# Performance work log

Measured on AMD Instinct MI355X. Metric: run time of the kernel, lower is better.

Reference implementation:

```python
import math
import jax, jax.numpy as jnp
import numpy as np

jax.config.update("jax_enable_x64", True)  # hash math uses int64, as in the torch reference

N_LEVELS = 16
F = 2                     # n_feat_per_entry
T = 2 ** 19               # hashmap size per level (max)
BASE_RES = 16
MAX_RES = 512
MIN_XYZ = -0.75           # origin (0,0,0), side 1.5
MAX_XYZ = 0.75
B = 1_000_000

# per_level_scale computed in float32 like torch.exp(torch.log(...))
_SCALE = float(np.exp(np.log(np.float32(MAX_RES / BASE_RES)) / np.float32(N_LEVELS - 1)))

def _level_info():
    offsets, res, n = [], [], 0
    for i in range(N_LEVELS):
        offsets.append(n)
        r = math.floor(BASE_RES * _SCALE ** i)
        res.append(r)
        n += min(T, (r + 1) ** 3)
    offsets.append(n)
    return offsets, res, n

OFFSETS, RES, N_TOTAL = _level_info()  # N_TOTAL == 5262476
PRIMES = np.array([1, 2654435761, 805459861], dtype=np.int64)
# corner offsets in {0,1}^3; weight = prod over dims of (frac if corner==1 else 1-frac)
CORNERS = np.array([[i, j, k] for i in (0, 1) for j in (0, 1) for k in (0, 1)], dtype=np.int64)  # (8,3)


def _hashgrid_forward(xyz, embeddings):
    """xyz: (B,3) float32 inside the bbox; embeddings: (N_TOTAL,F) float32."""
    norm = (xyz - MIN_XYZ) / (MAX_XYZ - MIN_XYZ)  # (B,3) in [0,1]
    corners = jnp.asarray(CORNERS)                # (8,3) int64
    primes = jnp.asarray(PRIMES)                  # (3,) int64
    corner_is_one = jnp.asarray(CORNERS.astype(bool))  # (8,3)
    outs = [xyz]  # include_input=True, raw input first
    for lvl in range(N_LEVELS):
        r = RES[lvl]
        off = OFFSETS[lvl]
        size = OFFSETS[lvl + 1] - off   # = min(T, (r+1)^3)
        pos = norm * r                                     # (B,3)
        base = jnp.clip(jnp.floor(pos).astype(jnp.int64), 0, r - 1)  # (B,3)
        frac = pos - base.astype(pos.dtype)                # (B,3)
        idx3 = base[:, None, :] + corners[None]            # (B,8,3) grid-pt coords
        # fast_hash: xor of coord*prime per dim, then mod level size, plus level offset
        p = idx3 * primes                                  # (B,8,3) int64
        hidx = (p[..., 0] ^ p[..., 1] ^ p[..., 2]) % size + off  # (B,8)
        vals = embeddings[hidx]                            # (B,8,F) gather
        w = jnp.prod(jnp.where(corner_is_one[None], frac[:, None, :], 1.0 - frac[:, None, :]), axis=-1)  # (B,8)
        outs.append(jnp.einsum('bc,bcf->bf', w, vals))     # trilinear interp -> (B,F)
    return jnp.concatenate(outs, axis=-1)                  # (B, 3 + L*F) = (B,35)


def setup_inputs() -> dict:
    key = jax.random.key(0)
    k1, k2 = jax.random.split(key)
    # points strictly inside the bbox [-0.75, 0.75]^3
    xyz = jax.random.uniform(k1, (B, 3), dtype=jnp.float32,
                             minval=MIN_XYZ + 1e-3, maxval=MAX_XYZ - 1e-3)
    # torch init is uniform(-1e-4, 1e-4)
    emb = jax.random.uniform(k2, (N_TOTAL, F), dtype=jnp.float32, minval=-1e-4, maxval=1e-4)
    return {"xyz": xyz, "embeddings": emb}


def reference(xyz, embeddings):
    return _hashgrid_forward(xyz, embeddings)
```

## Files before the change

### kernel.cpp

```cpp
#include <hip/hip_runtime.h>
#include <stdint.h>
#include <string.h>

#define NLEV 16

typedef float  vfloat4 __attribute__((ext_vector_type(4)));

__device__ __forceinline__ void norm_coords(const float* __restrict__ xyz, int p,
                                            float& nx, float& ny, float& nz) {
    const float x = __builtin_nontemporal_load(xyz + 3 * p + 0);
    const float y = __builtin_nontemporal_load(xyz + 3 * p + 1);
    const float z = __builtin_nontemporal_load(xyz + 3 * p + 2);
    const float inv = 1.0f / 1.5f;
    nx = (x + 0.75f) * inv;
    ny = (y + 0.75f) * inv;
    nz = (z + 0.75f) * inv;
}

__device__ __forceinline__ float2 trilerp(const float2 v[8],
                                          float fx, float fy, float fz) {
    const float gx = 1.0f - fx, gy = 1.0f - fy, gz = 1.0f - fz;
    const float w00 = gx * gy, w01 = gx * fy, w10 = fx * gy, w11 = fx * fy;
    float w, f0, f1;
    w = w00 * gz; f0 = w * v[0].x;          f1 = w * v[0].y;
    w = w00 * fz; f0 = fmaf(w, v[1].x, f0); f1 = fmaf(w, v[1].y, f1);
    w = w01 * gz; f0 = fmaf(w, v[2].x, f0); f1 = fmaf(w, v[2].y, f1);
    w = w01 * fz; f0 = fmaf(w, v[3].x, f0); f1 = fmaf(w, v[3].y, f1);
    w = w10 * gz; f0 = fmaf(w, v[4].x, f0); f1 = fmaf(w, v[4].y, f1);
    w = w10 * fz; f0 = fmaf(w, v[5].x, f0); f1 = fmaf(w, v[5].y, f1);
    w = w11 * gz; f0 = fmaf(w, v[6].x, f0); f1 = fmaf(w, v[6].y, f1);
    w = w11 * fz; f0 = fmaf(w, v[7].x, f0); f1 = fmaf(w, v[7].y, f1);
    return make_float2(f0, f1);
}

template<int R, uint32_t OFF>
__global__ __launch_bounds__(256, 4) void big_level2(
    const float* __restrict__ xyz,
    const float2* __restrict__ emb,
    float2* __restrict__ ws,
    int nb)
{
    const int t  = threadIdx.x;
    const int p0 = blockIdx.x * 512 + t;
    const int p1 = p0 + 256;
    const int q[2] = { p0 < nb ? p0 : nb - 1, p1 < nb ? p1 : nb - 1 };

    const float4* __restrict__ emb4 = (const float4*)emb;
    const uint32_t M = 524287u;

    uint32_t h0[2][4];
    uint32_t yzs[2][4];
    uint32_t hx1_[2];
    float4   V[2][4];
    float2   w1[2][4];
    float    fx[2], fy[2], fz[2];
    bool     oddbx[2];

    #pragma unroll
    for (int j = 0; j < 2; ++j) {
        float nx, ny, nz;
        norm_coords(xyz, q[j], nx, ny, nz);
        const float rf = (float)R;
        const float px = nx * rf, py = ny * rf, pz = nz * rf;
        int bx = (int)floorf(px); bx = bx < 0 ? 0 : (bx > R - 1 ? R - 1 : bx);
        int by = (int)floorf(py); by = by < 0 ? 0 : (by > R - 1 ? R - 1 : by);
        int bz = (int)floorf(pz); bz = bz < 0 ? 0 : (bz > R - 1 ? R - 1 : bz);
        fx[j] = px - (float)bx;
        fy[j] = py - (float)by;
        fz[j] = pz - (float)bz;

        const uint32_t hy0 = (uint32_t)by       * 2654435761u;
        const uint32_t hy1 = (uint32_t)(by + 1) * 2654435761u;
        const uint32_t hz0 = (uint32_t)bz       * 805459861u;
        const uint32_t hz1 = (uint32_t)(bz + 1) * 805459861u;
        yzs[j][0] = hy0 ^ hz0; yzs[j][1] = hy0 ^ hz1;
        yzs[j][2] = hy1 ^ hz0; yzs[j][3] = hy1 ^ hz1;

        const uint32_t hx0 = (uint32_t)bx;
        oddbx[j] = (bx & 1) != 0;
        hx1_[j]  = hx0 + 1u;

        #pragma unroll
        for (int i = 0; i < 4; ++i) {
            h0[j][i] = (hx0 ^ yzs[j][i]) & M;
            V[j][i]  = emb4[(h0[j][i] >> 1) + (OFF >> 1)];
        }
    }

    #pragma unroll
    for (int j = 0; j < 2; ++j) {
        if (oddbx[j]) {
            #pragma unroll
            for (int i = 0; i < 4; ++i)
                w1[j][i] = emb[((hx1_[j] ^ yzs[j][i]) & M) + OFF];
        }
    }

    float2 r[2];
    #pragma unroll
    for (int j = 0; j < 2; ++j) {
        float2 v[8];
        #pragma unroll
        for (int i = 0; i < 4; ++i) {
            const float2 lo = make_float2(V[j][i].x, V[j][i].y);
            const float2 hi = make_float2(V[j][i].z, V[j][i].w);
            const bool oh = (h0[j][i] & 1u) != 0u;
            v[i]     = oh ? hi : lo;
            v[i + 4] = oddbx[j] ? w1[j][i] : (oh ? lo : hi);
        }
        r[j] = trilerp(v, fx[j], fy[j], fz[j]);
    }

    uint64_t u0, u1;
    memcpy(&u0, &r[0], 8);
    memcpy(&u1, &r[1], 8);
    if (p0 < nb) __builtin_nontemporal_store(u0, (uint64_t*)ws + p0);
    if (p1 < nb) __builtin_nontemporal_store(u1, (uint64_t*)ws + p1);
}

__global__ __launch_bounds__(256, 4) void pack_small(
    const float* __restrict__ xyz,
    const float2* __restrict__ emb,
    const float2* __restrict__ ws,
    float* __restrict__ out,
    int nb)
{
    constexpr int      kRes[7]  = {16, 20, 25, 32, 40, 50, 64};
    constexpr uint32_t kSize[7] = {4913u, 9261u, 17576u, 35937u, 68921u, 132651u, 274625u};
    constexpr uint32_t kOff[7]  = {0u, 4913u, 14174u, 31750u, 67687u, 136608u, 269259u};

    __shared__ __align__(16) float lds[4 * 64 * 35];

    const int tid  = threadIdx.x;
    const int lane = tid & 63;
    const int wid  = tid >> 6;
    const int p    = blockIdx.x * 256 + tid;
    const int pc   = (p < nb) ? p : (nb - 1);

    uint64_t wsv[9];
    #pragma unroll
    for (int l = 0; l < 9; ++l)
        wsv[l] = __builtin_nontemporal_load(
            (const uint64_t*)ws + (size_t)l * nb + pc);

    const float x = xyz[3 * pc + 0];
    const float y = xyz[3 * pc + 1];
    const float z = xyz[3 * pc + 2];

    float* wl = &lds[(wid * 64 + lane) * 35];
    wl[0] = x; wl[1] = y; wl[2] = z;

    const float inv = 1.0f / 1.5f;
    const float nx = (x + 0.75f) * inv;
    const float ny = (y + 0.75f) * inv;
    const float nz = (z + 0.75f) * inv;

    uint32_t idx[2][8];
    float2   v[2][8];
    float    fr[2][3];

    auto level_idx = [&](int lv, uint32_t (&ix)[8], float (&f)[3]) {
        const int      r   = kRes[lv];
        const float    rf  = (float)r;
        const uint32_t sz  = kSize[lv];
        const uint32_t off = kOff[lv];

        const float px = nx * rf, py = ny * rf, pz = nz * rf;
        int bx = (int)floorf(px); bx = bx < 0 ? 0 : (bx > r - 1 ? r - 1 : bx);
        int by = (int)floorf(py); by = by < 0 ? 0 : (by > r - 1 ? r - 1 : by);
        int bz = (int)floorf(pz); bz = bz < 0 ? 0 : (bz > r - 1 ? r - 1 : bz);
        f[0] = px - (float)bx;
        f[1] = py - (float)by;
        f[2] = pz - (float)bz;

        const uint64_t hx0 = (uint64_t)(uint32_t)bx;
        const uint64_t hx1 = hx0 + 1u;
        const uint64_t hy0 = (uint64_t)(uint32_t)by       * 2654435761ull;
        const uint64_t hy1 = (uint64_t)(uint32_t)(by + 1) * 2654435761ull;
        const uint64_t hz0 = (uint64_t)(uint32_t)bz       * 805459861ull;
        const uint64_t hz1 = (uint64_t)(uint32_t)(bz + 1) * 805459861ull;

        const uint64_t yz00 = hy0 ^ hz0, yz01 = hy0 ^ hz1;
        const uint64_t yz10 = hy1 ^ hz0, yz11 = hy1 ^ hz1;

        ix[0] = (uint32_t)((hx0 ^ yz00) % sz) + off;
        ix[1] = (uint32_t)((hx0 ^ yz01) % sz) + off;
        ix[2] = (uint32_t)((hx0 ^ yz10) % sz) + off;
        ix[3] = (uint32_t)((hx0 ^ yz11) % sz) + off;
        ix[4] = (uint32_t)((hx1 ^ yz00) % sz) + off;
        ix[5] = (uint32_t)((hx1 ^ yz01) % sz) + off;
        ix[6] = (uint32_t)((hx1 ^ yz10) % sz) + off;
        ix[7] = (uint32_t)((hx1 ^ yz11) % sz) + off;
    };

    level_idx(0, idx[0], fr[0]);
    #pragma unroll
    for (int i = 0; i < 8; ++i) v[0][i] = emb[idx[0][i]];

    #pragma unroll
    for (int l = 0; l < 7; ++l) {
        const int cur = l & 1;
        const int nxt = cur ^ 1;
        if (l < 6) {
            level_idx(l + 1, idx[nxt], fr[nxt]);
            #pragma unroll
            for (int i = 0; i < 8; ++i) v[nxt][i] = emb[idx[nxt][i]];
        }
        const float2 rr = trilerp(v[cur], fr[cur][0], fr[cur][1], fr[cur][2]);
        wl[3 + 2 * l] = rr.x;
        wl[4 + 2 * l] = rr.y;
    }

    #pragma unroll
    for (int l = 0; l < 9; ++l) {
        float2 bv;
        memcpy(&bv, &wsv[l], 8);
        wl[3 + 2 * (l + 7)] = bv.x;
        wl[4 + 2 * (l + 7)] = bv.y;
    }

    __syncthreads();

    const int wave_gid = blockIdx.x * 4 + wid;
    if (wave_gid * 64 < nb) {
        const vfloat4* s4 = (const vfloat4*)&lds[wid * 64 * 35];
        vfloat4* d4 = (vfloat4*)(out + (size_t)wave_gid * (64 * 35));
        #pragma unroll
        for (int c = 0; c < 8; ++c)
            __builtin_nontemporal_store(s4[c * 64 + lane], &d4[c * 64 + lane]);
        if (lane < 48)
            __builtin_nontemporal_store(s4[8 * 64 + lane], &d4[8 * 64 + lane]);
    }
}

__global__ __launch_bounds__(256, 4) void hashgrid_mono(
    const float* __restrict__ xyz,
    const float2* __restrict__ emb,
    float* __restrict__ out,
    int nb)
{
    constexpr int      kRes[NLEV]  = {16,20,25,32,40,50,64,80,101,128,161,203,256,322,406,512};
    constexpr uint32_t kSize[NLEV] = {4913u,9261u,17576u,35937u,68921u,132651u,274625u,
                                      524288u,524288u,524288u,524288u,524288u,
                                      524288u,524288u,524288u,524288u};
    constexpr uint32_t kOff[NLEV]  = {0u,4913u,14174u,31750u,67687u,136608u,269259u,543884u,
                                      1068172u,1592460u,2116748u,2641036u,3165324u,
                                      3689612u,4213900u,4738188u};

    __shared__ __align__(16) float lds[4 * 64 * 35];

    const int tid  = threadIdx.x;
    const int lane = tid & 63;
    const int wid  = tid >> 6;
    const int p    = blockIdx.x * 256 + tid;
    const int pc   = (p < nb) ? p : (nb - 1);

    const float x = xyz[3 * pc + 0];
    const float y = xyz[3 * pc + 1];
    const float z = xyz[3 * pc + 2];

    float* wl = &lds[(wid * 64 + lane) * 35];
    wl[0] = x; wl[1] = y; wl[2] = z;

    const float inv = 1.0f / 1.5f;
    const float nx = (x + 0.75f) * inv;
    const float ny = (y + 0.75f) * inv;
    const float nz = (z + 0.75f) * inv;

    #pragma unroll
    for (int l = 0; l < NLEV; ++l) {
        const int      r   = kRes[l];
        const float    rf  = (float)r;
        const uint32_t sz  = kSize[l];
        const uint32_t off = kOff[l];

        const float px = nx * rf, py = ny * rf, pz = nz * rf;
        int bx = (int)floorf(px); bx = bx < 0 ? 0 : (bx > r - 1 ? r - 1 : bx);
        int by = (int)floorf(py); by = by < 0 ? 0 : (by > r - 1 ? r - 1 : by);
        int bz = (int)floorf(pz); bz = bz < 0 ? 0 : (bz > r - 1 ? r - 1 : bz);
        const float fx = px - (float)bx;
        const float fy = py - (float)by;
        const float fz = pz - (float)bz;

        const uint64_t hx0 = (uint64_t)(uint32_t)bx;
        const uint64_t hx1 = hx0 + 1u;
        const uint64_t hy0 = (uint64_t)(uint32_t)by       * 2654435761ull;
        const uint64_t hy1 = (uint64_t)(uint32_t)(by + 1) * 2654435761ull;
        const uint64_t hz0 = (uint64_t)(uint32_t)bz       * 805459861ull;
        const uint64_t hz1 = (uint64_t)(uint32_t)(bz + 1) * 805459861ull;

        const uint64_t yz00 = hy0 ^ hz0, yz01 = hy0 ^ hz1;
        const uint64_t yz10 = hy1 ^ hz0, yz11 = hy1 ^ hz1;

        const uint32_t i000 = (uint32_t)((hx0 ^ yz00) % sz) + off;
        const uint32_t i001 = (uint32_t)((hx0 ^ yz01) % sz) + off;
        const uint32_t i010 = (uint32_t)((hx0 ^ yz10) % sz) + off;
        const uint32_t i011 = (uint32_t)((hx0 ^ yz11) % sz) + off;
        const uint32_t i100 = (uint32_t)((hx1 ^ yz00) % sz) + off;
        const uint32_t i101 = (uint32_t)((hx1 ^ yz01) % sz) + off;
        const uint32_t i110 = (uint32_t)((hx1 ^ yz10) % sz) + off;
        const uint32_t i111 = (uint32_t)((hx1 ^ yz11) % sz) + off;

        const float2 v000 = emb[i000];
        const float2 v001 = emb[i001];
        const float2 v010 = emb[i010];
        const float2 v011 = emb[i011];
        const float2 v100 = emb[i100];
        const float2 v101 = emb[i101];
        const float2 v110 = emb[i110];
        const float2 v111 = emb[i111];

        const float gx = 1.0f - fx, gy = 1.0f - fy, gz = 1.0f - fz;
        const float w00 = gx * gy, w01 = gx * fy, w10 = fx * gy, w11 = fx * fy;

        float w, f0, f1;
        w = w00 * gz; f0 = w * v000.x;          f1 = w * v000.y;
        w = w00 * fz; f0 = fmaf(w, v001.x, f0); f1 = fmaf(w, v001.y, f1);
        w = w01 * gz; f0 = fmaf(w, v010.x, f0); f1 = fmaf(w, v010.y, f1);
        w = w01 * fz; f0 = fmaf(w, v011.x, f0); f1 = fmaf(w, v011.y, f1);
        w = w10 * gz; f0 = fmaf(w, v100.x, f0); f1 = fmaf(w, v100.y, f1);
        w = w10 * fz; f0 = fmaf(w, v101.x, f0); f1 = fmaf(w, v101.y, f1);
        w = w11 * gz; f0 = fmaf(w, v110.x, f0); f1 = fmaf(w, v110.y, f1);
        w = w11 * fz; f0 = fmaf(w, v111.x, f0); f1 = fmaf(w, v111.y, f1);

        wl[3 + 2 * l] = f0;
        wl[4 + 2 * l] = f1;
    }

    __syncthreads();

    const int wave_gid = blockIdx.x * 4 + wid;
    if (wave_gid * 64 < nb) {
        const float* src = &lds[wid * 64 * 35];
        float* dst = out + (size_t)wave_gid * (64 * 35);
        #pragma unroll
        for (int c = 0; c < 35; ++c)
            dst[c * 64 + lane] = src[c * 64 + lane];
    }
}

extern "C" void kernel_launch(void* const* d_in, const int* in_sizes, int n_in,
                              void* d_out, int out_size, void* d_ws, size_t ws_size,
                              hipStream_t stream) {
    const float*  xyz = (const float*)d_in[0];
    const float2* emb = (const float2*)d_in[1];
    float*        out = (float*)d_out;
    const int nb = in_sizes[0] / 3;
    const int blocks  = (nb + 255) / 256;
    const int blocks2 = (nb + 511) / 512;

    const size_t ws_need = (size_t)9 * (size_t)nb * sizeof(float2);
    if (ws_size < ws_need) {
        hashgrid_mono<<<blocks, 256, 0, stream>>>(xyz, emb, out, nb);
        return;
    }

    float2* ws = (float2*)d_ws;
    big_level2< 80,  543884u><<<blocks2, 256, 0, stream>>>(xyz, emb, ws + (size_t)0 * nb, nb);
    big_level2<101, 1068172u><<<blocks2, 256, 0, stream>>>(xyz, emb, ws + (size_t)1 * nb, nb);
    big_level2<128, 1592460u><<<blocks2, 256, 0, stream>>>(xyz, emb, ws + (size_t)2 * nb, nb);
    big_level2<161, 2116748u><<<blocks2, 256, 0, stream>>>(xyz, emb, ws + (size_t)3 * nb, nb);
    big_level2<203, 2641036u><<<blocks2, 256, 0, stream>>>(xyz, emb, ws + (size_t)4 * nb, nb);
    big_level2<256, 3165324u><<<blocks2, 256, 0, stream>>>(xyz, emb, ws + (size_t)5 * nb, nb);
    big_level2<322, 3689612u><<<blocks2, 256, 0, stream>>>(xyz, emb, ws + (size_t)6 * nb, nb);
    big_level2<406, 4213900u><<<blocks2, 256, 0, stream>>>(xyz, emb, ws + (size_t)7 * nb, nb);
    big_level2<512, 4738188u><<<blocks2, 256, 0, stream>>>(xyz, emb, ws + (size_t)8 * nb, nb);
    pack_small<<<blocks, 256, 0, stream>>>(xyz, emb, ws, out, nb);
}
```

Measured before the change: 625.2 us.

## Process four points per thread in big-level kernels and deepen small-level prefetch

```diff
diff --git a/kernel.cpp b/kernel.cpp
--- a/kernel.cpp
+++ b/kernel.cpp
@@ -33,92 +33,112 @@
     return make_float2(f0, f1);
 }
 
+struct BigPt {
+    uint32_t h0[4];
+    uint32_t yzs[4];
+    uint32_t hx1;
+    bool     oddbx;
+    float    fx, fy, fz;
+    float4   V[4];
+    float2   w1[4];
+};
+
 template<int R, uint32_t OFF>
-__global__ __launch_bounds__(256, 4) void big_level2(
+__device__ __forceinline__ void big_issue(const float4* __restrict__ emb4,
+                                          const float2* __restrict__ emb,
+                                          float nx, float ny, float nz, BigPt& s) {
+    const uint32_t M = 524287u;
+    const float rf = (float)R;
+    const float px = nx * rf, py = ny * rf, pz = nz * rf;
+    int bx = (int)floorf(px); bx = bx < 0 ? 0 : (bx > R - 1 ? R - 1 : bx);
+    int by = (int)floorf(py); by = by < 0 ? 0 : (by > R - 1 ? R - 1 : by);
+    int bz = (int)floorf(pz); bz = bz < 0 ? 0 : (bz > R - 1 ? R - 1 : bz);
+    s.fx = px - (float)bx;
+    s.fy = py - (float)by;
+    s.fz = pz - (float)bz;
+
+    const uint32_t hy0 = (uint32_t)by       * 2654435761u;
+    const uint32_t hy1 = (uint32_t)(by + 1) * 2654435761u;
+    const uint32_t hz0 = (uint32_t)bz       * 805459861u;
+    const uint32_t hz1 = (uint32_t)(bz + 1) * 805459861u;
+    s.yzs[0] = hy0 ^ hz0; s.yzs[1] = hy0 ^ hz1;
+    s.yzs[2] = hy1 ^ hz0; s.yzs[3] = hy1 ^ hz1;
+
+    const uint32_t hx0 = (uint32_t)bx;
+    s.oddbx = (bx & 1) != 0;
+    s.hx1   = hx0 + 1u;
+
+    #pragma unroll
+    for (int i = 0; i < 4; ++i) {
+        s.h0[i] = (hx0 ^ s.yzs[i]) & M;
+        s.V[i]  = emb4[(s.h0[i] >> 1) + (OFF >> 1)];
+    }
+    if (s.oddbx) {
+        #pragma unroll
+        for (int i = 0; i < 4; ++i)
+            s.w1[i] = emb[((s.hx1 ^ s.yzs[i]) & M) + OFF];
+    }
+}
+
+__device__ __forceinline__ float2 big_consume(const BigPt& s) {
+    float2 v[8];
+    #pragma unroll
+    for (int i = 0; i < 4; ++i) {
+        const float2 lo = make_float2(s.V[i].x, s.V[i].y);
+        const float2 hi = make_float2(s.V[i].z, s.V[i].w);
+        const bool oh = (s.h0[i] & 1u) != 0u;
+        v[i]     = oh ? hi : lo;
+        v[i + 4] = s.oddbx ? s.w1[i] : (oh ? lo : hi);
+    }
+    return trilerp(v, s.fx, s.fy, s.fz);
+}
+
+template<int R, uint32_t OFF>
+__global__ __launch_bounds__(256, 4) void big_level4(
     const float* __restrict__ xyz,
     const float2* __restrict__ emb,
     float2* __restrict__ ws,
     int nb)
 {
-    const int t  = threadIdx.x;
-    const int p0 = blockIdx.x * 512 + t;
-    const int p1 = p0 + 256;
-    const int q[2] = { p0 < nb ? p0 : nb - 1, p1 < nb ? p1 : nb - 1 };
-
+    const int t    = threadIdx.x;
+    const int base = blockIdx.x * 1024 + t;
     const float4* __restrict__ emb4 = (const float4*)emb;
-    const uint32_t M = 524287u;
-
-    uint32_t h0[2][4];
-    uint32_t yzs[2][4];
-    uint32_t hx1_[2];
-    float4   V[2][4];
-    float2   w1[2][4];
-    float    fx[2], fy[2], fz[2];
-    bool     oddbx[2];
-
-    #pragma unroll
-    for (int j = 0; j < 2; ++j) {
-        float nx, ny, nz;
-        norm_coords(xyz, q[j], nx, ny, nz);
-        const float rf = (float)R;
-        const float px = nx * rf, py = ny * rf, pz = nz * rf;
-        int bx = (int)floorf(px); bx = bx < 0 ? 0 : (bx > R - 1 ? R - 1 : bx);
-        int by = (int)floorf(py); by = by < 0 ? 0 : (by > R - 1 ? R - 1 : by);
-        int bz = (int)floorf(pz); bz = bz < 0 ? 0 : (bz > R - 1 ? R - 1 : bz);
-        fx[j] = px - (float)bx;
-        fy[j] = py - (float)by;
-        fz[j] = pz - (float)bz;
-
-        const uint32_t hy0 = (uint32_t)by       * 2654435761u;
-        const uint32_t hy1 = (uint32_t)(by + 1) * 2654435761u;
-        const uint32_t hz0 = (uint32_t)bz       * 805459861u;
-        const uint32_t hz1 = (uint32_t)(bz + 1) * 805459861u;
-        yzs[j][0] = hy0 ^ hz0; yzs[j][1] = hy0 ^ hz1;
-        yzs[j][2] = hy1 ^ hz0; yzs[j][3] = hy1 ^ hz1;
-
-        const uint32_t hx0 = (uint32_t)bx;
-        oddbx[j] = (bx & 1) != 0;
-        hx1_[j]  = hx0 + 1u;
-
-        #pragma unroll
-        for (int i = 0; i < 4; ++i) {
-            h0[j][i] = (hx0 ^ yzs[j][i]) & M;
-            V[j][i]  = emb4[(h0[j][i] >> 1) + (OFF >> 1)];
-        }
-    }
-
-    #pragma unroll
-    for (int j = 0; j < 2; ++j) {
-        if (oddbx[j]) {
-            #pragma unroll
-            for (int i = 0; i < 4; ++i)
-                w1[j][i] = emb[((hx1_[j] ^ yzs[j][i]) & M) + OFF];
-        }
-    }
-
-    float2 r[2];
-    #pragma unroll
-    for (int j = 0; j < 2; ++j) {
-        float2 v[8];
-        #pragma unroll
-        for (int i = 0; i < 4; ++i) {
-            const float2 lo = make_float2(V[j][i].x, V[j][i].y);
-            const float2 hi = make_float2(V[j][i].z, V[j][i].w);
-            const bool oh = (h0[j][i] & 1u) != 0u;
-            v[i]     = oh ? hi : lo;
-            v[i + 4] = oddbx[j] ? w1[j][i] : (oh ? lo : hi);
-        }
-        r[j] = trilerp(v, fx[j], fy[j], fz[j]);
-    }
-
-    uint64_t u0, u1;
-    memcpy(&u0, &r[0], 8);
-    memcpy(&u1, &r[1], 8);
+
+    int p0 = base, p1 = base + 256, p2 = base + 512, p3 = base + 768;
+    const int q0 = p0 < nb ? p0 : nb - 1;
+    const int q1 = p1 < nb ? p1 : nb - 1;
+    const int q2 = p2 < nb ? p2 : nb - 1;
+    const int q3 = p3 < nb ? p3 : nb - 1;
+
+    float nx0, ny0, nz0, nx1, ny1, nz1, nx2, ny2, nz2, nx3, ny3, nz3;
+    norm_coords(xyz, q0, nx0, ny0, nz0);
+    norm_coords(xyz, q1, nx1, ny1, nz1);
+    norm_coords(xyz, q2, nx2, ny2, nz2);
+    norm_coords(xyz, q3, nx3, ny3, nz3);
+
+    BigPt s0, s1, s2, s3;
+    big_issue<R, OFF>(emb4, emb, nx0, ny0, nz0, s0);
+    big_issue<R, OFF>(emb4, emb, nx1, ny1, nz1, s1);
+    big_issue<R, OFF>(emb4, emb, nx2, ny2, nz2, s2);
+
+    const float2 r0 = big_consume(s0);
+    big_issue<R, OFF>(emb4, emb, nx3, ny3, nz3, s3);
+    const float2 r1 = big_consume(s1);
+    const float2 r2 = big_consume(s2);
+    const float2 r3 = big_consume(s3);
+
+    uint64_t u0, u1, u2, u3;
+    memcpy(&u0, &r0, 8);
+    memcpy(&u1, &r1, 8);
+    memcpy(&u2, &r2, 8);
+    memcpy(&u3, &r3, 8);
     if (p0 < nb) __builtin_nontemporal_store(u0, (uint64_t*)ws + p0);
     if (p1 < nb) __builtin_nontemporal_store(u1, (uint64_t*)ws + p1);
-}
-
-__global__ __launch_bounds__(256, 4) void pack_small(
+    if (p2 < nb) __builtin_nontemporal_store(u2, (uint64_t*)ws + p2);
+    if (p3 < nb) __builtin_nontemporal_store(u3, (uint64_t*)ws + p3);
+}
+
+__global__ __launch_bounds__(64, 4) void pack_small(
     const float* __restrict__ xyz,
     const float2* __restrict__ emb,
     const float2* __restrict__ ws,
@@ -129,12 +149,10 @@
     constexpr uint32_t kSize[7] = {4913u, 9261u, 17576u, 35937u, 68921u, 132651u, 274625u};
     constexpr uint32_t kOff[7]  = {0u, 4913u, 14174u, 31750u, 67687u, 136608u, 269259u};
 
-    __shared__ __align__(16) float lds[4 * 64 * 35];
-
-    const int tid  = threadIdx.x;
-    const int lane = tid & 63;
-    const int wid  = tid >> 6;
-    const int p    = blockIdx.x * 256 + tid;
+    __shared__ __align__(16) float lds[64 * 35];
+
+    const int lane = threadIdx.x;
+    const int p    = blockIdx.x * 64 + lane;
     const int pc   = (p < nb) ? p : (nb - 1);
 
     uint64_t wsv[9];
@@ -147,7 +165,7 @@
     const float y = xyz[3 * pc + 1];
     const float z = xyz[3 * pc + 2];
 
-    float* wl = &lds[(wid * 64 + lane) * 35];
+    float* wl = &lds[lane * 35];
     wl[0] = x; wl[1] = y; wl[2] = z;
 
     const float inv = 1.0f / 1.5f;
@@ -155,9 +173,9 @@
     const float ny = (y + 0.75f) * inv;
     const float nz = (z + 0.75f) * inv;
 
-    uint32_t idx[2][8];
-    float2   v[2][8];
-    float    fr[2][3];
+    uint32_t idx[3][8];
+    float2   v[3][8];
+    float    fr[3][3];
 
     auto level_idx = [&](int lv, uint32_t (&ix)[8], float (&f)[3]) {
         const int      r   = kRes[lv];
@@ -196,13 +214,16 @@
     level_idx(0, idx[0], fr[0]);
     #pragma unroll
     for (int i = 0; i < 8; ++i) v[0][i] = emb[idx[0][i]];
+    level_idx(1, idx[1], fr[1]);
+    #pragma unroll
+    for (int i = 0; i < 8; ++i) v[1][i] = emb[idx[1][i]];
 
     #pragma unroll
     for (int l = 0; l < 7; ++l) {
-        const int cur = l & 1;
-        const int nxt = cur ^ 1;
-        if (l < 6) {
-            level_idx(l + 1, idx[nxt], fr[nxt]);
+        const int cur = l % 3;
+        if (l < 5) {
+            const int nxt = (l + 2) % 3;
+            level_idx(l + 2, idx[nxt], fr[nxt]);
             #pragma unroll
             for (int i = 0; i < 8; ++i) v[nxt][i] = emb[idx[nxt][i]];
         }
@@ -221,10 +242,9 @@
 
     __syncthreads();
 
-    const int wave_gid = blockIdx.x * 4 + wid;
-    if (wave_gid * 64 < nb) {
-        const vfloat4* s4 = (const vfloat4*)&lds[wid * 64 * 35];
-        vfloat4* d4 = (vfloat4*)(out + (size_t)wave_gid * (64 * 35));
+    if (blockIdx.x * 64 < nb) {
+        const vfloat4* s4 = (const vfloat4*)lds;
+        vfloat4* d4 = (vfloat4*)(out + (size_t)blockIdx.x * (64 * 35));
         #pragma unroll
         for (int c = 0; c < 8; ++c)
             __builtin_nontemporal_store(s4[c * 64 + lane], &d4[c * 64 + lane]);
@@ -346,24 +366,25 @@
     const float2* emb = (const float2*)d_in[1];
     float*        out = (float*)d_out;
     const int nb = in_sizes[0] / 3;
-    const int blocks  = (nb + 255) / 256;
-    const int blocks2 = (nb + 511) / 512;
+    const int blocksP = (nb + 63) / 64;
+    const int blocksB = (nb + 1023) / 1024;
 
     const size_t ws_need = (size_t)9 * (size_t)nb * sizeof(float2);
     if (ws_size < ws_need) {
-        hashgrid_mono<<<blocks, 256, 0, stream>>>(xyz, emb, out, nb);
+        const int blocksM = (nb + 255) / 256;
+        hashgrid_mono<<<blocksM, 256, 0, stream>>>(xyz, emb, out, nb);
         return;
     }
 
     float2* ws = (float2*)d_ws;
-    big_level2< 80,  543884u><<<blocks2, 256, 0, stream>>>(xyz, emb, ws + (size_t)0 * nb, nb);
-    big_level2<101, 1068172u><<<blocks2, 256, 0, stream>>>(xyz, emb, ws + (size_t)1 * nb, nb);
-    big_level2<128, 1592460u><<<blocks2, 256, 0, stream>>>(xyz, emb, ws + (size_t)2 * nb, nb);
-    big_level2<161, 2116748u><<<blocks2, 256, 0, stream>>>(xyz, emb, ws + (size_t)3 * nb, nb);
-    big_level2<203, 2641036u><<<blocks2, 256, 0, stream>>>(xyz, emb, ws + (size_t)4 * nb, nb);
-    big_level2<256, 3165324u><<<blocks2, 256, 0, stream>>>(xyz, emb, ws + (size_t)5 * nb, nb);
-    big_level2<322, 3689612u><<<blocks2, 256, 0, stream>>>(xyz, emb, ws + (size_t)6 * nb, nb);
-    big_level2<406, 4213900u><<<blocks2, 256, 0, stream>>>(xyz, emb, ws + (size_t)7 * nb, nb);
-    big_level2<512, 4738188u><<<blocks2, 256, 0, stream>>>(xyz, emb, ws + (size_t)8 * nb, nb);
-    pack_small<<<blocks, 256, 0, stream>>>(xyz, emb, ws, out, nb);
-}
+    big_level4< 80,  543884u><<<blocksB, 256, 0, stream>>>(xyz, emb, ws + (size_t)0 * nb, nb);
+    big_level4<101, 1068172u><<<blocksB, 256, 0, stream>>>(xyz, emb, ws + (size_t)1 * nb, nb);
+    big_level4<128, 1592460u><<<blocksB, 256, 0, stream>>>(xyz, emb, ws + (size_t)2 * nb, nb);
+    big_level4<161, 2116748u><<<blocksB, 256, 0, stream>>>(xyz, emb, ws + (size_t)3 * nb, nb);
+    big_level4<203, 2641036u><<<blocksB, 256, 0, stream>>>(xyz, emb, ws + (size_t)4 * nb, nb);
+    big_level4<256, 3165324u><<<blocksB, 256, 0, stream>>>(xyz, emb, ws + (size_t)5 * nb, nb);
+    big_level4<322, 3689612u><<<blocksB, 256, 0, stream>>>(xyz, emb, ws + (size_t)6 * nb, nb);
+    big_level4<406, 4213900u><<<blocksB, 256, 0, stream>>>(xyz, emb, ws + (size_t)7 * nb, nb);
+    big_level4<512, 4738188u><<<blocksB, 256, 0, stream>>>(xyz, emb, ws + (size_t)8 * nb, nb);
+    pack_small<<<blocksP, 64, 0, stream>>>(xyz, emb, ws, out, nb);
+}
```

Result: slower. 732.9 us (+17.2%).

## Pair x-adjacent hash corners into one 16-byte load for dense levels

Applied to the files above, without the earlier changes.

```diff
diff --git a/kernel.cpp b/kernel.cpp
--- a/kernel.cpp
+++ b/kernel.cpp
@@ -155,24 +155,22 @@
     const float ny = (y + 0.75f) * inv;
     const float nz = (z + 0.75f) * inv;
 
-    uint32_t idx[2][8];
-    float2   v[2][8];
-    float    fr[2][3];
-
-    auto level_idx = [&](int lv, uint32_t (&ix)[8], float (&f)[3]) {
-        const int      r   = kRes[lv];
+    #pragma unroll
+    for (int l = 0; l < 7; ++l) {
+        const int      r   = kRes[l];
         const float    rf  = (float)r;
-        const uint32_t sz  = kSize[lv];
-        const uint32_t off = kOff[lv];
+        const uint32_t sz  = kSize[l];
+        const uint32_t off = kOff[l];
 
         const float px = nx * rf, py = ny * rf, pz = nz * rf;
         int bx = (int)floorf(px); bx = bx < 0 ? 0 : (bx > r - 1 ? r - 1 : bx);
         int by = (int)floorf(py); by = by < 0 ? 0 : (by > r - 1 ? r - 1 : by);
         int bz = (int)floorf(pz); bz = bz < 0 ? 0 : (bz > r - 1 ? r - 1 : bz);
-        f[0] = px - (float)bx;
-        f[1] = py - (float)by;
-        f[2] = pz - (float)bz;
-
+        const float fx = px - (float)bx;
+        const float fy = py - (float)by;
+        const float fz = pz - (float)bz;
+
+        const bool     evenbx = (bx & 1) == 0;
         const uint64_t hx0 = (uint64_t)(uint32_t)bx;
         const uint64_t hx1 = hx0 + 1u;
         const uint64_t hy0 = (uint64_t)(uint32_t)by       * 2654435761ull;
@@ -180,33 +178,30 @@
         const uint64_t hz0 = (uint64_t)(uint32_t)bz       * 805459861ull;
         const uint64_t hz1 = (uint64_t)(uint32_t)(bz + 1) * 805459861ull;
 
-        const uint64_t yz00 = hy0 ^ hz0, yz01 = hy0 ^ hz1;
-        const uint64_t yz10 = hy1 ^ hz0, yz11 = hy1 ^ hz1;
-
-        ix[0] = (uint32_t)((hx0 ^ yz00) % sz) + off;
-        ix[1] = (uint32_t)((hx0 ^ yz01) % sz) + off;
-        ix[2] = (uint32_t)((hx0 ^ yz10) % sz) + off;
-        ix[3] = (uint32_t)((hx0 ^ yz11) % sz) + off;
-        ix[4] = (uint32_t)((hx1 ^ yz00) % sz) + off;
-        ix[5] = (uint32_t)((hx1 ^ yz01) % sz) + off;
-        ix[6] = (uint32_t)((hx1 ^ yz10) % sz) + off;
-        ix[7] = (uint32_t)((hx1 ^ yz11) % sz) + off;
-    };
-
-    level_idx(0, idx[0], fr[0]);
-    #pragma unroll
-    for (int i = 0; i < 8; ++i) v[0][i] = emb[idx[0][i]];
-
-    #pragma unroll
-    for (int l = 0; l < 7; ++l) {
-        const int cur = l & 1;
-        const int nxt = cur ^ 1;
-        if (l < 6) {
-            level_idx(l + 1, idx[nxt], fr[nxt]);
-            #pragma unroll
-            for (int i = 0; i < 8; ++i) v[nxt][i] = emb[idx[nxt][i]];
+        const uint64_t yzc[4] = { hy0 ^ hz0, hy0 ^ hz1, hy1 ^ hz0, hy1 ^ hz1 };
+
+        float2 v[8];
+        #pragma unroll
+        for (int c = 0; c < 4; ++c) {
+            const uint64_t a0 = hx0 ^ yzc[c];
+            const uint32_t h0 = (uint32_t)(a0 % sz);
+            const bool     odd_a = ((uint32_t)a0 & 1u) != 0u;
+            const int  hm = (int)h0 - (int)(odd_a ? 1 : 0);
+            const bool ok = evenbx && (hm >= 0) && (hm != (int)sz - 1);
+            const uint32_t iload = (ok ? (uint32_t)hm : h0) + off;
+            const float4 V = *(const float4*)(emb + iload);
+            float2 w1 = make_float2(0.0f, 0.0f);
+            if (!ok) {
+                const uint32_t h1 = (uint32_t)((hx1 ^ yzc[c]) % sz);
+                w1 = emb[h1 + off];
+            }
+            const float2 loV = make_float2(V.x, V.y);
+            const float2 hiV = make_float2(V.z, V.w);
+            v[c]     = ok ? (odd_a ? hiV : loV) : loV;
+            v[c + 4] = ok ? (odd_a ? loV : hiV) : w1;
         }
-        const float2 rr = trilerp(v[cur], fr[cur][0], fr[cur][1], fr[cur][2]);
+
+        const float2 rr = trilerp(v, fx, fy, fz);
         wl[3 + 2 * l] = rr.x;
         wl[4 + 2 * l] = rr.y;
     }
```

Measured after the change: 584.7 us. 6.5% less time.
